# Optimization experiments

Measured on AMD Instinct MI355X. Metric: run time of the kernel, lower is better.

## Reference

```python
import jax, jax.numpy as jnp
import numpy as np

B, S, DIM = 4, 2048, 2048
H, KVH, HD = 32, 8, 64
REPEATS = H // KVH
SCALE = HD ** -0.5


def _rope(x, cos, sin):
    # x: (B, S, Hn, HD); cos/sin: (S, HD//2)
    xr = x[..., 0::2]
    xi = x[..., 1::2]
    c = cos[:, None, :]  # (S, 1, HD//2) broadcasts over heads
    s = sin[:, None, :]
    out_r = xr * c - xi * s
    out_i = xr * s + xi * c
    return jnp.stack([out_r, out_i], axis=-1).reshape(x.shape)


def setup_inputs() -> dict:
    key = jax.random.key(0)
    ks = jax.random.split(key, 5)
    x = jax.random.normal(ks[0], (B, S, DIM), dtype=jnp.float32)
    wq = jax.random.normal(ks[1], (H * HD, DIM), dtype=jnp.float32) * 0.02
    wk = jax.random.normal(ks[2], (KVH * HD, DIM), dtype=jnp.float32) * 0.02
    wv = jax.random.normal(ks[3], (KVH * HD, DIM), dtype=jnp.float32) * 0.02
    wo = jax.random.normal(ks[4], (DIM, H * HD), dtype=jnp.float32) * 0.02
    # standard RoPE frequencies: freqs_cis = exp(i * t * theta)
    inv_freq = 1.0 / (10000.0 ** (jnp.arange(0, HD, 2, dtype=jnp.float32) / HD))
    angles = jnp.arange(S, dtype=jnp.float32)[:, None] * inv_freq[None, :]  # (S, HD//2)
    return {
        "x": x, "wq": wq, "wk": wk, "wv": wv, "wo": wo,
        "freqs_cos": jnp.cos(angles), "freqs_sin": jnp.sin(angles),
    }


def reference(x, wq, wk, wv, wo, freqs_cos, freqs_sin):
    b, s, _ = x.shape
    q = (x @ wq.T).reshape(b, s, H, HD)
    k = (x @ wk.T).reshape(b, s, KVH, HD)
    v = (x @ wv.T).reshape(b, s, KVH, HD)
    q = _rope(q, freqs_cos, freqs_sin)
    k = _rope(k, freqs_cos, freqs_sin)
    k_rep = jnp.repeat(k, REPEATS, axis=2)  # (B,S,H,HD)
    v_rep = jnp.repeat(v, REPEATS, axis=2)
    # NOTE: faithful to source - q is NOT transposed to (B,H,S,HD), so the
    # matmul contracts head_dim at each token, producing (B,S,H,H) scores
    # (mixing across heads per position), softmaxed over the last head axis.
    scores = jnp.einsum('bshd,bsed->bshe', q, k_rep) * SCALE  # (B,S,H,H)
    weights = jax.nn.softmax(scores, axis=-1)
    out = jnp.einsum('bshe,bsed->bshd', weights, v_rep)  # (B,S,H,HD)
    out = out.reshape(b, s, H * HD)
    return out @ wo.T
```

## Files before the change

### kernel.cpp

```cpp
#include <hip/hip_runtime.h>

typedef unsigned short u16;
typedef __bf16 bf16x8 __attribute__((ext_vector_type(8)));
typedef float f32x4 __attribute__((ext_vector_type(4)));

#define AS1 __attribute__((address_space(1)))
#define AS3 __attribute__((address_space(3)))

__device__ inline u16 f2bf(float f) {
    union { float f; unsigned u; } c; c.f = f;
    unsigned u = c.u;
    u += 0x7fffu + ((u >> 16) & 1u);
    return (u16)(u >> 16);
}
__device__ inline float bf2f(u16 b) {
    union { unsigned u; float f; } c; c.u = ((unsigned)b) << 16;
    return c.f;
}

__device__ inline void async_cp16(const void* g, void* l) {
    __builtin_amdgcn_global_load_lds((const AS1 void*)g, (AS3 void*)l, 16, 0, 0);
}

__global__ __launch_bounds__(256)
void conv_all(const float* __restrict__ x,
              const float* __restrict__ wq, const float* __restrict__ wk,
              const float* __restrict__ wv, const float* __restrict__ wo,
              u16* __restrict__ x_bf, u16* __restrict__ wqkv,
              u16* __restrict__ wo_bf) {
    int b = blockIdx.x;
    if (b < 8192) {
        int i = (b * 256 + threadIdx.x) * 8;
        float4 f0 = *(const float4*)(x + i);
        float4 f1 = *(const float4*)(x + i + 4);
        union { u16 h[8]; uint4 v; } o;
        o.h[0] = f2bf(f0.x); o.h[1] = f2bf(f0.y);
        o.h[2] = f2bf(f0.z); o.h[3] = f2bf(f0.w);
        o.h[4] = f2bf(f1.x); o.h[5] = f2bf(f1.y);
        o.h[6] = f2bf(f1.z); o.h[7] = f2bf(f1.w);
        *(uint4*)(x_bf + i) = o.v;
    } else {
        int i = ((b - 8192) * 256 + threadIdx.x) * 4;
        const float* src;
        u16* dst;
        if (i < 4194304)       { src = wq + i;           dst = wqkv + i; }
        else if (i < 5242880)  { src = wk + (i-4194304); dst = wqkv + i; }
        else if (i < 6291456)  { src = wv + (i-5242880); dst = wqkv + i; }
        else                   { src = wo + (i-6291456); dst = wo_bf + (i-6291456); }
        float4 f = *(const float4*)src;
        union { u16 h[4]; uint2 v; } o;
        o.h[0] = f2bf(f.x); o.h[1] = f2bf(f.y);
        o.h[2] = f2bf(f.z); o.h[3] = f2bf(f.w);
        *(uint2*)dst = o.v;
    }
}

template <int NI, bool BF16_OUT>
__global__ __launch_bounds__(512, 2)
void gemm_bt8(const u16* __restrict__ A, const u16* __restrict__ B,
              void* __restrict__ Cout, int N, int K) {
    constexpr int SZ = 32768 + NI * 8192;
    __shared__ __align__(16) char ldsc[2 * SZ];

    const int tid  = threadIdx.x;
    const int w    = tid >> 6;
    const int lane = tid & 63;
    const int row0 = blockIdx.x * 256;
    const int col0 = blockIdx.y * (NI * 64);
    const int wm = w >> 2, wn = w & 3;
    const int lm = lane & 15, quad = lane >> 4;

    const int NT  = K / 64;
    const int NIT = K / 128;
    const int K64 = K * 64;

    const int sr  = lane >> 3;
    const int stC = ((lane & 7) ^ sr) * 8;
    const u16* pA = A + (size_t)(row0 + w * 8 + sr) * K + stC;
    const u16* pB = B + (size_t)(col0 + w * 8 + sr) * K + stC;
    const int stagoff = w * 1024;

    const int cx0   = (quad ^ (lm & 7)) * 16;
    const int cx1   = cx0 ^ 64;
    const int aBase = (wm * 128 + lm) * 128;
    const int bBase = 32768 + (wn * (NI * 16) + lm) * 128;

    f32x4 acc[8][NI];
#pragma unroll
    for (int i = 0; i < 8; i++)
#pragma unroll
        for (int j = 0; j < NI; j++) acc[i][j] = (f32x4){0.f, 0.f, 0.f, 0.f};

    auto stage = [&](const u16* base, int v, int unit, int regionOff) {
        int kb = (v < NT ? v : NT - 1) * 64;
        async_cp16(base + (size_t)unit * K64 + kb,
                   ldsc + (v & 1) * SZ + regionOff + unit * 8192 + stagoff);
    };
#define ST_A(v, u) stage(pA, (v), (u), 0)
#define ST_B(v, u) stage(pB, (v), (u), 32768)

#pragma unroll
    for (int u = 0; u < 4; u++) ST_A(0, u);
#pragma unroll
    for (int u = 0; u < NI; u++) ST_B(0, u);
#pragma unroll
    for (int u = 0; u < NI; u++) ST_B(1, u);
    ST_A(1, 0); ST_A(1, 1);
    if constexpr (NI == 4) asm volatile("s_waitcnt vmcnt(6)" ::: "memory");
    else                   asm volatile("s_waitcnt vmcnt(5)" ::: "memory");
    __builtin_amdgcn_s_barrier();

    bf16x8 bg[NI][2], afX[2][2], afY[2][2];

#define LDR(off) (*(const bf16x8*)(ldsc + (off)))

#define PHASE_TAIL(MI0, AF)                                                   \
    __builtin_amdgcn_s_barrier();                                             \
    asm volatile("s_waitcnt lgkmcnt(0)" ::: "memory");                        \
    __builtin_amdgcn_sched_barrier(0);                                        \
    __builtin_amdgcn_s_setprio(1);                                            \
    _Pragma("unroll")                                                         \
    for (int s = 0; s < 2; s++)                                               \
        _Pragma("unroll")                                                     \
        for (int j = 0; j < 2; j++)                                           \
            _Pragma("unroll")                                                 \
            for (int ni = 0; ni < NI; ni++)                                   \
                acc[(MI0) + j][ni] = __builtin_amdgcn_mfma_f32_16x16x32_bf16( \
                    AF[j][s], bg[ni][s], acc[(MI0) + j][ni], 0, 0, 0);        \
    __builtin_amdgcn_s_setprio(0);

#define HALF_ITER(u, BO)                                                      \
    {                                                                         \
                                                                      \
        _Pragma("unroll")                                                     \
        for (int ni = 0; ni < NI; ni++) {                                     \
            bg[ni][0] = LDR((BO) + bBase + ni * 2048 + cx0);                  \
            bg[ni][1] = LDR((BO) + bBase + ni * 2048 + cx1);                  \
        }                                                                     \
        _Pragma("unroll")                                                     \
        for (int j = 0; j < 2; j++) {                                         \
            afX[j][0] = LDR((BO) + aBase + j * 2048 + cx0);                   \
            afX[j][1] = LDR((BO) + aBase + j * 2048 + cx1);                   \
            afY[j][0] = LDR((BO) + aBase + (2 + j) * 2048 + cx0);             \
            afY[j][1] = LDR((BO) + aBase + (2 + j) * 2048 + cx1);             \
        }                                                                     \
        ST_A((u) + 1, 2); ST_A((u) + 1, 3);                                   \
        asm volatile("s_waitcnt lgkmcnt(8)" ::: "memory");                    \
        PHASE_TAIL(0, afX)                                                    \
        __builtin_amdgcn_s_barrier();                                         \
                                                                      \
        _Pragma("unroll")                                                     \
        for (int j = 0; j < 2; j++) {                                         \
            afX[j][0] = LDR((BO) + aBase + (4 + j) * 2048 + cx0);             \
            afX[j][1] = LDR((BO) + aBase + (4 + j) * 2048 + cx1);             \
        }                                                                     \
        ST_B((u) + 2, 0); ST_B((u) + 2, 1);                                   \
        PHASE_TAIL(2, afY)                                                    \
        __builtin_amdgcn_s_barrier();                                         \
                                                                      \
        _Pragma("unroll")                                                     \
        for (int j = 0; j < 2; j++) {                                         \
            afY[j][0] = LDR((BO) + aBase + (6 + j) * 2048 + cx0);             \
            afY[j][1] = LDR((BO) + aBase + (6 + j) * 2048 + cx1);             \
        }                                                                     \
        ST_B((u) + 2, 2);                                                     \
        if constexpr (NI == 4) { ST_B((u) + 2, 3); }                          \
        else                   { ST_A((u) + 2, 0); }                          \
        PHASE_TAIL(4, afX)                                                    \
        __builtin_amdgcn_s_barrier();                                         \
                                                                      \
        if constexpr (NI == 4) { ST_A((u) + 2, 0); ST_A((u) + 2, 1); }        \
        else                   { ST_A((u) + 2, 1); }                          \
        PHASE_TAIL(6, afY)                                                    \
        if constexpr (NI == 4) asm volatile("s_waitcnt vmcnt(6)" ::: "memory");\
        else                   asm volatile("s_waitcnt vmcnt(5)" ::: "memory");\
        __builtin_amdgcn_s_barrier();                                         \
    }

    for (int it = 0; it < NIT; ++it) {
        const int t = 2 * it;
        HALF_ITER(t, 0)
        HALF_ITER(t + 1, SZ)
    }

#undef HALF_ITER
#undef PHASE_TAIL
#undef LDR
#undef ST_A
#undef ST_B

    const int rbase = row0 + wm * 128 + quad * 4;
    const int cbase = col0 + wn * (NI * 16) + lm;
    if (BF16_OUT) {
        u16* C = (u16*)Cout;
#pragma unroll
        for (int mi = 0; mi < 8; mi++)
#pragma unroll
            for (int r = 0; r < 4; r++) {
                size_t ro = (size_t)(rbase + mi * 16 + r) * N;
#pragma unroll
                for (int ni = 0; ni < NI; ni++)
                    C[ro + cbase + ni * 16] = f2bf(acc[mi][ni][r]);
            }
    } else {
        float* C = (float*)Cout;
#pragma unroll
        for (int mi = 0; mi < 8; mi++)
#pragma unroll
            for (int r = 0; r < 4; r++) {
                size_t ro = (size_t)(rbase + mi * 16 + r) * N;
#pragma unroll
                for (int ni = 0; ni < NI; ni++)
                    C[ro + cbase + ni * 16] = acc[mi][ni][r];
            }
    }
}

__global__ __launch_bounds__(256)
void attn_tok(const u16* __restrict__ qkv, u16* __restrict__ out) {
    __shared__ float kvf[1024];
    const int tok = blockIdx.x;
    const int t = threadIdx.x;
    const u16* qrow = qkv + (size_t)tok * 3072;

    {
        uint2 w = *(const uint2*)(qrow + 2048 + t * 4);
        kvf[t * 4 + 0] = bf2f((u16)(w.x & 0xffff));
        kvf[t * 4 + 1] = bf2f((u16)(w.x >> 16));
        kvf[t * 4 + 2] = bf2f((u16)(w.y & 0xffff));
        kvf[t * 4 + 3] = bf2f((u16)(w.y >> 16));
    }
    __syncthreads();

    const int h = t >> 3, j = t & 7;
    float qf[8];
    {
        uint4 w = *(const uint4*)(qrow + h * 64 + j * 8);
        unsigned ws4[4] = {w.x, w.y, w.z, w.w};
#pragma unroll
        for (int i = 0; i < 4; i++) {
            qf[2 * i]     = bf2f((u16)(ws4[i] & 0xffff));
            qf[2 * i + 1] = bf2f((u16)(ws4[i] >> 16));
        }
    }

    float s[8];
#pragma unroll
    for (int g = 0; g < 8; g++) {
        const float* kk = kvf + g * 64 + j * 8;
        float a = 0.f;
#pragma unroll
        for (int d = 0; d < 8; d++) a += qf[d] * kk[d];
        s[g] = a;
    }
#pragma unroll
    for (int g = 0; g < 8; g++) {
        s[g] += __shfl_xor(s[g], 1);
        s[g] += __shfl_xor(s[g], 2);
        s[g] += __shfl_xor(s[g], 4);
    }
    float m = -1e30f;
#pragma unroll
    for (int g = 0; g < 8; g++) { s[g] *= 0.125f; m = fmaxf(m, s[g]); }
    float p[8], l = 0.f;
#pragma unroll
    for (int g = 0; g < 8; g++) { p[g] = __expf(s[g] - m); l += p[g]; }
    float rl = 1.f / l;

    float o[8] = {0, 0, 0, 0, 0, 0, 0, 0};
#pragma unroll
    for (int g = 0; g < 8; g++) {
        float w = p[g] * rl;
        const float* vv = kvf + 512 + g * 64 + j * 8;
#pragma unroll
        for (int d = 0; d < 8; d++) o[d] += w * vv[d];
    }

    unsigned po[4];
#pragma unroll
    for (int i = 0; i < 4; i++)
        po[i] = (unsigned)f2bf(o[2 * i]) | ((unsigned)f2bf(o[2 * i + 1]) << 16);
    uint4 wo_; wo_.x = po[0]; wo_.y = po[1]; wo_.z = po[2]; wo_.w = po[3];
    *(uint4*)(out + (size_t)tok * 2048 + h * 64 + j * 8) = wo_;
}

extern "C" void kernel_launch(void* const* d_in, const int* in_sizes, int n_in,
                              void* d_out, int out_size, void* d_ws, size_t ws_size,
                              hipStream_t stream) {
    const float* x  = (const float*)d_in[0];
    const float* wq = (const float*)d_in[1];
    const float* wk = (const float*)d_in[2];
    const float* wv = (const float*)d_in[3];
    const float* wo = (const float*)d_in[4];

    u16* x_bf  = (u16*)d_ws;
    u16* wqkv  = x_bf  + 16777216;
    u16* wo_bf = wqkv  + 6291456;
    u16* qkv   = wo_bf + 4194304;
    u16* attn  = qkv   + 25165824;

    conv_all<<<18432, dim3(256), 0, stream>>>(x, wq, wk, wv, wo, x_bf, wqkv, wo_bf);

    gemm_bt8<3, true><<<dim3(32, 16), dim3(512), 0, stream>>>(x_bf, wqkv, qkv,
                                                              3072, 2048);

    attn_tok<<<8192, dim3(256), 0, stream>>>(qkv, attn);

    gemm_bt8<4, false><<<dim3(32, 8), dim3(512), 0, stream>>>(attn, wo_bf,
                                                              (float*)d_out,
                                                              2048, 2048);
}
```

Measured before the change: 328.9 us.

## Software-pipeline LDS fragment reads across GEMM phases and reuse x_bf buffer for attention

Restructures the GEMM main loop so A fragments for the next phase, and for NI==3 the B fragments for the next k-tile, are read from LDS before the current phase's MFMAs run. It adds sched_barriers and finer lgkmcnt waits so LDS reads overlap MFMA work, and it double-buffers the B fragment registers. The global-to-LDS staging order and the vmcnt thresholds are rebalanced to match. The attention output now reuses the x_bf workspace region, which shrinks the workspace footprint but relies on x_bf being dead after the QKV GEMM.

After: 319.2 us. -2.9%, faster.

```diff
diff --git a/kernel.cpp b/kernel.cpp
--- a/kernel.cpp
+++ b/kernel.cpp
@@ -99,25 +99,24 @@
 #define ST_A(v, u) stage(pA, (v), (u), 0)
 #define ST_B(v, u) stage(pB, (v), (u), 32768)
 
-#pragma unroll
-    for (int u = 0; u < 4; u++) ST_A(0, u);
-#pragma unroll
-    for (int u = 0; u < NI; u++) ST_B(0, u);
-#pragma unroll
-    for (int u = 0; u < NI; u++) ST_B(1, u);
-    ST_A(1, 0); ST_A(1, 1);
-    if constexpr (NI == 4) asm volatile("s_waitcnt vmcnt(6)" ::: "memory");
-    else                   asm volatile("s_waitcnt vmcnt(5)" ::: "memory");
-    __builtin_amdgcn_s_barrier();
-
-    bf16x8 bg[NI][2], afX[2][2], afY[2][2];
-
 #define LDR(off) (*(const bf16x8*)(ldsc + (off)))
-
-#define PHASE_TAIL(MI0, AF)                                                   \
-    __builtin_amdgcn_s_barrier();                                             \
-    asm volatile("s_waitcnt lgkmcnt(0)" ::: "memory");                        \
-    __builtin_amdgcn_sched_barrier(0);                                        \
+#define SB __builtin_amdgcn_sched_barrier(0)
+#define BAR __builtin_amdgcn_s_barrier()
+#define WLG(n) asm volatile("s_waitcnt lgkmcnt(" #n ")" ::: "memory")
+
+#define RD_AF(DST, BASEOFF, MIBASE)                                           \
+    _Pragma("unroll")                                                         \
+    for (int j = 0; j < 2; j++) {                                             \
+        DST[j][0] = LDR((BASEOFF) + aBase + ((MIBASE) + j) * 2048 + cx0);     \
+        DST[j][1] = LDR((BASEOFF) + aBase + ((MIBASE) + j) * 2048 + cx1);     \
+    }
+#define RD_BG(DST, BASEOFF)                                                   \
+    _Pragma("unroll")                                                         \
+    for (int ni = 0; ni < NI; ni++) {                                         \
+        DST[ni][0] = LDR((BASEOFF) + bBase + ni * 2048 + cx0);                \
+        DST[ni][1] = LDR((BASEOFF) + bBase + ni * 2048 + cx1);                \
+    }
+#define MFMA_TAIL(MI0, AF, BG)                                                \
     __builtin_amdgcn_s_setprio(1);                                            \
     _Pragma("unroll")                                                         \
     for (int s = 0; s < 2; s++)                                               \
@@ -126,65 +125,92 @@
             _Pragma("unroll")                                                 \
             for (int ni = 0; ni < NI; ni++)                                   \
                 acc[(MI0) + j][ni] = __builtin_amdgcn_mfma_f32_16x16x32_bf16( \
-                    AF[j][s], bg[ni][s], acc[(MI0) + j][ni], 0, 0, 0);        \
+                    AF[j][s], BG[ni][s], acc[(MI0) + j][ni], 0, 0, 0);        \
     __builtin_amdgcn_s_setprio(0);
 
-#define HALF_ITER(u, BO)                                                      \
+    bf16x8 bgA[NI][2], bgB[NI][2], F[2][2], G[2][2];
+
+#pragma unroll
+    for (int u = 0; u < 4; u++) ST_A(0, u);
+#pragma unroll
+    for (int u = 0; u < NI; u++) ST_B(0, u);
+#pragma unroll
+    for (int u = 0; u < NI; u++) ST_B(1, u);
+    ST_A(1, 0);
+    if constexpr (NI == 3) asm volatile("s_waitcnt vmcnt(4)" ::: "memory");
+    else                   asm volatile("s_waitcnt vmcnt(5)" ::: "memory");
+    SB;
+    if constexpr (NI == 3) { RD_BG(bgA, 0) }
+    RD_AF(F, 0, 0)
+    SB;
+    BAR;
+
+#define HALF_ITER(u, BO, BN, BGC, BGN)                                        \
     {                                                                         \
                                                                       \
-        _Pragma("unroll")                                                     \
-        for (int ni = 0; ni < NI; ni++) {                                     \
-            bg[ni][0] = LDR((BO) + bBase + ni * 2048 + cx0);                  \
-            bg[ni][1] = LDR((BO) + bBase + ni * 2048 + cx1);                  \
-        }                                                                     \
-        _Pragma("unroll")                                                     \
-        for (int j = 0; j < 2; j++) {                                         \
-            afX[j][0] = LDR((BO) + aBase + j * 2048 + cx0);                   \
-            afX[j][1] = LDR((BO) + aBase + j * 2048 + cx1);                   \
-            afY[j][0] = LDR((BO) + aBase + (2 + j) * 2048 + cx0);             \
-            afY[j][1] = LDR((BO) + aBase + (2 + j) * 2048 + cx1);             \
-        }                                                                     \
-        ST_A((u) + 1, 2); ST_A((u) + 1, 3);                                   \
-        asm volatile("s_waitcnt lgkmcnt(8)" ::: "memory");                    \
-        PHASE_TAIL(0, afX)                                                    \
-        __builtin_amdgcn_s_barrier();                                         \
+        if constexpr (NI == 4) { RD_BG(BGC, BO) }                             \
+        SB;                                                                   \
+        RD_AF(G, BO, 2)                                                       \
+        SB;                                                                   \
+        ST_A((u) + 1, 1); ST_A((u) + 1, 2); ST_A((u) + 1, 3);                 \
+        SB;                                                                   \
+        BAR;                                                                  \
+        WLG(4);                                                               \
+        SB;                                                                   \
+        MFMA_TAIL(0, F, BGC)                                                  \
+        SB;                                                                   \
+        BAR;                                                                  \
                                                                       \
-        _Pragma("unroll")                                                     \
-        for (int j = 0; j < 2; j++) {                                         \
-            afX[j][0] = LDR((BO) + aBase + (4 + j) * 2048 + cx0);             \
-            afX[j][1] = LDR((BO) + aBase + (4 + j) * 2048 + cx1);             \
-        }                                                                     \
+        RD_AF(F, BO, 4)                                                       \
+        SB;                                                                   \
         ST_B((u) + 2, 0); ST_B((u) + 2, 1);                                   \
-        PHASE_TAIL(2, afY)                                                    \
-        __builtin_amdgcn_s_barrier();                                         \
+        SB;                                                                   \
+        BAR;                                                                  \
+        WLG(4);                                                               \
+        SB;                                                                   \
+        MFMA_TAIL(2, G, BGC)                                                  \
+        SB;                                                                   \
+        BAR;                                                                  \
                                                                       \
-        _Pragma("unroll")                                                     \
-        for (int j = 0; j < 2; j++) {                                         \
-            afY[j][0] = LDR((BO) + aBase + (6 + j) * 2048 + cx0);             \
-            afY[j][1] = LDR((BO) + aBase + (6 + j) * 2048 + cx1);             \
-        }                                                                     \
+        RD_AF(G, BO, 6)                                                       \
+        SB;                                                                   \
         ST_B((u) + 2, 2);                                                     \
         if constexpr (NI == 4) { ST_B((u) + 2, 3); }                          \
-        else                   { ST_A((u) + 2, 0); }                          \
-        PHASE_TAIL(4, afX)                                                    \
-        __builtin_amdgcn_s_barrier();                                         \
-                                                                      \
-        if constexpr (NI == 4) { ST_A((u) + 2, 0); ST_A((u) + 2, 1); }        \
-        else                   { ST_A((u) + 2, 1); }                          \
-        PHASE_TAIL(6, afY)                                                    \
-        if constexpr (NI == 4) asm volatile("s_waitcnt vmcnt(6)" ::: "memory");\
+        ST_A((u) + 2, 0);                                                     \
+        SB;                                                                   \
+        BAR;                                                                  \
+        WLG(4);                                                               \
+        SB;                                                                   \
+        MFMA_TAIL(4, F, BGC)                                                  \
+        SB;                                                                   \
+        BAR;                                                                  \
+                               \
+        WLG(0);                                                               \
+        SB;                                                                   \
+        MFMA_TAIL(6, G, BGC)                                                  \
+        SB;                                                                   \
+        if constexpr (NI == 3) asm volatile("s_waitcnt vmcnt(4)" ::: "memory");\
         else                   asm volatile("s_waitcnt vmcnt(5)" ::: "memory");\
-        __builtin_amdgcn_s_barrier();                                         \
+        SB;                                                                   \
+        if constexpr (NI == 3) { RD_BG(BGN, BN) }                             \
+        RD_AF(F, BN, 0)                                                       \
+        SB;                                                                   \
+        BAR;                                                                  \
     }
 
     for (int it = 0; it < NIT; ++it) {
         const int t = 2 * it;
-        HALF_ITER(t, 0)
-        HALF_ITER(t + 1, SZ)
+        HALF_ITER(t, 0, SZ, bgA, bgB)
+        HALF_ITER(t + 1, SZ, 0, bgB, bgA)
     }
 
 #undef HALF_ITER
-#undef PHASE_TAIL
+#undef MFMA_TAIL
+#undef RD_BG
+#undef RD_AF
+#undef WLG
+#undef BAR
+#undef SB
 #undef LDR
 #undef ST_A
 #undef ST_B
@@ -297,7 +323,7 @@
     u16* wqkv  = x_bf  + 16777216;
     u16* wo_bf = wqkv  + 6291456;
     u16* qkv   = wo_bf + 4194304;
-    u16* attn  = qkv   + 25165824;
+    u16* attn  = x_bf;
 
     conv_all<<<18432, dim3(256), 0, stream>>>(x, wq, wk, wv, wo, x_bf, wqkv, wo_bf);
 
```
